# Optimization experiments

Measured on AMD Instinct MI355X. Metric: run time of the kernel, lower is better.

Reference implementation:

```python
import jax, jax.numpy as jnp
import numpy as np

N_SAMPLES = 32768
WS, STEP = 2048, 256
DILATIONS = (1, 2, 4, 8, 16, 32, 64, 1)
N_KEEP = 16
N_ROOMS = 8
N_ATOMS = 2048


def stft_mag(x):
    # x: (B, 1, N) -> magnitude spectrogram (B, 128, 1025)
    B = x.shape[0]
    xx = jnp.pad(x.reshape(B, -1), ((0, 0), (0, WS - STEP)))  # right-pad -> exactly N/STEP frames
    n_frames = N_SAMPLES // STEP  # 128
    idx = jnp.arange(n_frames)[:, None] * STEP + jnp.arange(WS)[None, :]
    frames = xx[:, idx] * jnp.hanning(WS)[None, None, :]  # (B, 128, 2048)
    return jnp.abs(jnp.fft.rfft(frames, axis=-1))


def fft_convolve(a, b):
    # linear convolution via zero-padding to 2N, sliced back to N
    n = a.shape[-1]
    pad = [(0, 0)] * (a.ndim - 1) + [(0, n)]
    sa = jnp.fft.rfft(jnp.pad(a, pad), axis=-1)
    sb = jnp.fft.rfft(jnp.pad(b, pad), axis=-1)
    return jnp.fft.irfft(sa * sb, n=2 * n, axis=-1)[..., :n]


def mlp(z, w, b, g, be, ow, ob):
    # LinearOutputStack: (Linear -> LayerNorm -> leaky_relu) x3 -> Linear
    for i in range(w.shape[0]):
        z = z @ w[i] + b[i]
        mu = jnp.mean(z, -1, keepdims=True)
        var = jnp.var(z, -1, keepdims=True)
        z = (z - mu) / jnp.sqrt(var + 1e-5) * g[i] + be[i]
        z = jax.nn.leaky_relu(z, 0.2)
    return z @ ow + ob


def setup_inputs() -> dict:
    key = jax.random.key(0)
    ks = jax.random.split(key, 12)
    s = 0.02
    B = 4
    decay = jnp.linspace(1.0, 0.0, N_SAMPLES) ** 2
    atoms = jax.random.uniform(ks[0], (N_ATOMS, N_SAMPLES), minval=-0.01, maxval=0.01) * decay[None, :]
    imp = jax.random.normal(ks[1], (N_ROOMS, N_SAMPLES)) * (jnp.linspace(1.0, 0.0, N_SAMPLES) ** 4)[None, :]
    imp = imp / jnp.linalg.norm(imp, axis=-1, keepdims=True)
    return {
        'x': jax.random.normal(ks[2], (B, 1, N_SAMPLES)),
        'atoms': atoms,
        'enc_w': jax.random.normal(ks[3], (8, 1024, 1024, 2)) * s,
        'enc_b': jnp.zeros((8, 1024)),
        'up_w': jax.random.normal(ks[4], (256, 1024)) * s,
        'up_b': jnp.zeros((256,)),
        'lat_w': jax.random.normal(ks[5], (1024, 16)) * s,
        'lat_b': jnp.zeros((16,)),
        'room_w': jax.random.normal(ks[6], (3, 16, 16)) * s,
        'room_b': jnp.zeros((3, 16)),
        'room_g': jnp.ones((3, 16)),
        'room_be': jnp.zeros((3, 16)),
        'room_ow': jax.random.normal(ks[7], (16, N_ROOMS)) * s,
        'room_ob': jnp.zeros((N_ROOMS,)),
        'mix_w': jax.random.normal(ks[8], (3, 16, 16)) * s,
        'mix_b': jnp.zeros((3, 16)),
        'mix_g': jnp.ones((3, 16)),
        'mix_be': jnp.zeros((3, 16)),
        'mix_ow': jax.random.normal(ks[9], (16, 1)) * s,
        'mix_ob': jnp.zeros((1,)),
        'impulses': imp,
    }


def reference(x, atoms, enc_w, enc_b, up_w, up_b, lat_w, lat_b,
              room_w, room_b, room_g, room_be, room_ow, room_ob,
              mix_w, mix_b, mix_g, mix_be, mix_ow, mix_ob, impulses):
    B = x.shape[0]
    # ---- encode ----
    spec = stft_mag(x)[..., :1024]                    # (B, 128, 1024)
    h = jnp.transpose(spec, (0, 2, 1))                # (B, 1024, 128)
    for i, d in enumerate(DILATIONS):                  # anti-causal dilated residual stack
        y = jnp.pad(h, ((0, 0), (0, 0), (0, d)))      # pad the FUTURE
        y = jax.lax.conv_general_dilated(y, enc_w[i], (1,), 'VALID', rhs_dilation=(d,),
                                         dimension_numbers=('NCH', 'OIH', 'NCH'))
        h = h + jax.nn.leaky_relu(y + enc_b[i][None, :, None], 0.2)
    z = jnp.mean(h, axis=-1)                          # (B, 1024)
    dense = z @ lat_w + lat_b                          # (B, 16)
    dense = dense / (jnp.linalg.norm(dense, axis=-1, keepdims=True) + 1e-8)  # unit_norm
    # ---- generate ----
    enc = jnp.einsum('bct,oc->bot', h, up_w) + up_b[None, :, None]  # 1x1 conv -> (B, 256, 128)
    full = jnp.zeros((B, 256, N_SAMPLES), enc.dtype).at[:, :, ::STEP].set(enc)
    # sparsify2: flattened top-k over (channel, time)
    flat = full.reshape(B, -1)
    vals, idx = jax.lax.top_k(flat, N_KEEP)           # (B, 16)
    ch = idx // N_SAMPLES                              # atom/channel index per event
    t = idx % N_SAMPLES                                # time index per event
    packed = jnp.zeros((B, N_KEEP, N_SAMPLES), full.dtype).at[
        jnp.arange(B)[:, None], jnp.arange(N_KEEP)[None, :], t].set(vals)
    subset = atoms[ch]                                 # gather -> (B, 16, 32768)
    events = fft_convolve(packed, subset)              # (B, 16, N)
    dry = jnp.sum(events, axis=1, keepdims=True)       # (B, 1, N)
    # ---- reverb ----
    room = jax.nn.softmax(mlp(dense, room_w, room_b, room_g, room_be, room_ow, room_ob), axis=-1)
    impulse = room @ impulses                          # (B, N)
    wet = fft_convolve(dry, impulse[:, None, :])
    mix = jax.nn.sigmoid(mlp(dense, mix_w, mix_b, mix_g, mix_be, mix_ow, mix_ob))[:, :, None]  # (B,1,1)
    return dry * mix + wet * (1.0 - mix)
```

## Files before the change

kernel.cpp:

```cpp
#include <hip/hip_runtime.h>
#include <hip/hip_bf16.h>
#include <math.h>

#define NSMP 32768
#define NFR 128
#define NCH 1024
#define NB 4

typedef __attribute__((ext_vector_type(8))) short short8;
typedef __attribute__((ext_vector_type(4))) float f32x4;
typedef unsigned short ushort;

__device__ __forceinline__ void split_bf(float v, ushort& h, ushort& l) {
  __hip_bfloat16 bh = __float2bfloat16(v);
  float r = v - __bfloat162float(bh);
  __hip_bfloat16 bl = __float2bfloat16(r);
  h = *reinterpret_cast<ushort*>(&bh);
  l = *reinterpret_cast<ushort*>(&bl);
}

__device__ __forceinline__ void gload_lds16(const ushort* g, ushort* l) {
  __builtin_amdgcn_global_load_lds((const __attribute__((address_space(1))) void*)g,
                                   (__attribute__((address_space(3))) void*)l, 16, 0, 0);
}

__global__ __launch_bounds__(256) void stft_kernel(const float* __restrict__ x,
                                                   float* __restrict__ h,
                                                   ushort* __restrict__ hTh,
                                                   ushort* __restrict__ hTl,
                                                   ushort* __restrict__ hTh1,
                                                   ushort* __restrict__ hTl1) {
  __shared__ float re[2048];
  __shared__ float im[2048];
  __shared__ float twr[1024];
  __shared__ float twi[1024];
  int bid = blockIdx.x;
  int b = bid >> 7;
  int f = bid & 127;
  int tid = threadIdx.x;
  const float TWO_PI = 6.28318530717958647692f;
  if (f < 64) {
    size_t pidx = ((size_t)b * 192 + 128 + f) * 1024 + tid * 4;
    uint2 z = {0u, 0u};
    *(uint2*)&hTh[pidx] = z;  *(uint2*)&hTl[pidx] = z;
    *(uint2*)&hTh1[pidx] = z; *(uint2*)&hTl1[pidx] = z;
  }
  for (int k = tid; k < 1024; k += 256) {
    float ang = -TWO_PI * (float)k / 2048.0f;
    float sn, cs;
    sincosf(ang, &sn, &cs);
    twr[k] = cs; twi[k] = sn;
  }
  for (int i = tid; i < 2048; i += 256) {
    int rev = (int)(__brev((unsigned)i) >> 21);
    int pos = f * 256 + rev;
    float v = (pos < NSMP) ? x[b * NSMP + pos] : 0.f;
    float w = 0.5f - 0.5f * cosf(TWO_PI * (float)rev / 2047.0f);
    re[i] = v * w;
    im[i] = 0.f;
  }
  __syncthreads();
  for (int s = 0; s < 11; ++s) {
    for (int q = 0; q < 4; ++q) {
      int bi = tid + q * 256;
      int half = 1 << s;
      int j = bi & (half - 1);
      int i0 = ((bi >> s) << (s + 1)) | j;
      int i1 = i0 + half;
      int ti = j << (10 - s);
      float cs = twr[ti], sn = twi[ti];
      float ur = re[i0], ui = im[i0];
      float vr = re[i1], vi = im[i1];
      float tr = vr * cs - vi * sn;
      float tti = vr * sn + vi * cs;
      re[i0] = ur + tr; im[i0] = ui + tti;
      re[i1] = ur - tr; im[i1] = ui - tti;
    }
    __syncthreads();
  }
  for (int k = tid; k < 1024; k += 256) {
    float m = sqrtf(re[k] * re[k] + im[k] * im[k]);
    h[(b * NCH + k) * NFR + f] = m;
    ushort hi, lo;
    split_bf(m, hi, lo);
    size_t tidx = ((size_t)b * 192 + f) * 1024 + k;
    hTh[tidx] = hi;
    hTl[tidx] = lo;
  }
}

__global__ __launch_bounds__(256) void wsplit_kernel(const float* __restrict__ encw,
                                                     ushort* __restrict__ w0h, ushort* __restrict__ w0l,
                                                     ushort* __restrict__ w1h, ushort* __restrict__ w1l) {
  size_t F = (size_t)blockIdx.x * 256 + threadIdx.x;
  float4 v = ((const float4*)encw)[F];
  size_t lo_idx = F >> 9;
  int c0 = (int)(F & 511) * 2;
  size_t base = lo_idx * 1024 + c0;
  ushort h0, l0, h1, l1;
  split_bf(v.x, h0, l0);
  split_bf(v.z, h1, l1);
  *(ushort2*)&w0h[base] = (ushort2){h0, h1};
  *(ushort2*)&w0l[base] = (ushort2){l0, l1};
  split_bf(v.y, h0, l0);
  split_bf(v.w, h1, l1);
  *(ushort2*)&w1h[base] = (ushort2){h0, h1};
  *(ushort2*)&w1l[base] = (ushort2){l0, l1};
}

__global__ __launch_bounds__(256) void conv_mfma(const ushort* __restrict__ hTh,
                                                 const ushort* __restrict__ hTl,
                                                 const ushort* __restrict__ w0h, const ushort* __restrict__ w0l,
                                                 const ushort* __restrict__ w1h, const ushort* __restrict__ w1l,
                                                 int D, float* __restrict__ yp) {
  __shared__ ushort lds[49152];
  int tid = threadIdx.x;
  int og = blockIdx.x * 128;
  int b = blockIdx.y;
  int s = blockIdx.z;
  int wid = tid >> 6, lane = tid & 63;
  int wr = (wid >> 1) * 64, wc = (wid & 1) * 64;
  int lr = lane & 15, lk = lane >> 4;
  int srow = lane >> 2;
  int sgr = ((lane & 3) ^ ((lane >> 3) & 3)) * 8;

  f32x4 acc[4][4];
#pragma unroll
  for (int m = 0; m < 4; ++m)
#pragma unroll
    for (int n = 0; n < 4; ++n) acc[m][n] = (f32x4){0.f, 0.f, 0.f, 0.f};

  const ushort* hb_h = hTh + (size_t)b * 192 * 1024;
  const ushort* hb_l = hTl + (size_t)b * 192 * 1024;

  auto stage = [&](int buf, int p) {
    const ushort* Wh = (p < 4) ? w0h : w1h;
    const ushort* Wl = (p < 4) ? w0l : w1l;
    int rowoff = (p < 4) ? 0 : D;
    int c0 = s * 128 + (p & 3) * 32 + sgr;
    ushort* dbase = &lds[buf * 16384 + wid * 4096];
#pragma unroll
    for (int j = 0; j < 8; ++j) {
      int row = j * 16 + srow;
      const ushort* src;
      if (wid == 0)      src = Wh   + (size_t)(og + row) * 1024 + c0;
      else if (wid == 1) src = Wl   + (size_t)(og + row) * 1024 + c0;
      else if (wid == 2) src = hb_h + (size_t)(rowoff + row) * 1024 + c0;
      else               src = hb_l + (size_t)(rowoff + row) * 1024 + c0;
      gload_lds16(src, dbase + j * 512);
    }
  };

  auto compute = [&](int buf) {
    const ushort* base = &lds[buf * 16384];
    short8 ah[4], al[4], bh[4], bl[4];
#pragma unroll
    for (int m = 0; m < 4; ++m) {
      int ar = wr + m * 16 + lr;
      int off = ar * 32 + ((lk ^ ((ar >> 1) & 3)) << 3);
      ah[m] = *(const short8*)&base[off];
      al[m] = *(const short8*)&base[4096 + off];
    }
#pragma unroll
    for (int n = 0; n < 4; ++n) {
      int br = wc + n * 16 + lr;
      int off = br * 32 + ((lk ^ ((br >> 1) & 3)) << 3);
      bh[n] = *(const short8*)&base[8192 + off];
      bl[n] = *(const short8*)&base[12288 + off];
    }
#pragma unroll
    for (int m = 0; m < 4; ++m)
#pragma unroll
      for (int n = 0; n < 4; ++n) {
        acc[m][n] = __builtin_amdgcn_mfma_f32_16x16x32_bf16(ah[m], bh[n], acc[m][n], 0, 0, 0);
        acc[m][n] = __builtin_amdgcn_mfma_f32_16x16x32_bf16(ah[m], bl[n], acc[m][n], 0, 0, 0);
        acc[m][n] = __builtin_amdgcn_mfma_f32_16x16x32_bf16(al[m], bh[n], acc[m][n], 0, 0, 0);
      }
  };

  stage(0, 0);
  stage(1, 1);
#pragma unroll
  for (int p = 0; p < 8; ++p) {
    if (p < 7) asm volatile("s_waitcnt vmcnt(8)" ::: "memory");
    else       asm volatile("s_waitcnt vmcnt(0)" ::: "memory");
    __builtin_amdgcn_s_barrier();
    if (p + 2 < 8) stage((p + 2) % 3, p + 2);
    compute(p % 3);
  }

  float* dst = yp + (size_t)(s * 4 + b) * 131072;
#pragma unroll
  for (int m = 0; m < 4; ++m)
#pragma unroll
    for (int n = 0; n < 4; ++n)
#pragma unroll
      for (int r = 0; r < 4; ++r) {
        int orow = og + wr + m * 16 + lk * 4 + r;
        int col = wc + n * 16 + lr;
        dst[orow * 128 + col] = acc[m][n][r];
      }
}

__global__ __launch_bounds__(256) void conv_epi(const float* __restrict__ yp,
                                                const float* __restrict__ hin,
                                                const float* __restrict__ bias,
                                                float* __restrict__ hout,
                                                ushort* __restrict__ hTh,
                                                ushort* __restrict__ hTl,
                                                float* __restrict__ zbuf) {
  __shared__ float T[16][132];
  int og = blockIdx.x * 16;
  int b = blockIdx.y;
  int tid = threadIdx.x;
#pragma unroll
  for (int j = 0; j < 8; ++j) {
    int flat = j * 256 + tid;
    int o = flat >> 7, t = flat & 127;
    size_t base = ((size_t)b * NCH + og + o) * NFR + t;
    float v = 0.f;
#pragma unroll
    for (int sl = 0; sl < 8; ++sl) v += yp[(size_t)sl * 524288 + base];
    v += bias[og + o];
    v = (v > 0.f) ? v : 0.2f * v;
    float r = hin[base] + v;
    hout[base] = r;
    T[o][t] = r;
  }
  __syncthreads();
  if (tid < 16) {
    float s = 0.f;
#pragma unroll 8
    for (int t = 0; t < 128; ++t) s += T[tid][t];
    zbuf[b * NCH + og + tid] = s * (1.f / 128.f);
  }
#pragma unroll
  for (int j = 0; j < 8; ++j) {
    int flat = j * 256 + tid;
    int t = flat >> 4, o = flat & 15;
    ushort hi, lo;
    split_bf(T[o][t], hi, lo);
    size_t tidx = ((size_t)b * 192 + t) * 1024 + og + o;
    hTh[tidx] = hi;
    hTl[tidx] = lo;
  }
}

template <int TAPS, int D, int KTOT, int SPLIT, int MROWS>
__global__ __launch_bounds__(256, 2) void gemm_f32(const float* __restrict__ hin,
                                                   const float* __restrict__ W,
                                                   float* __restrict__ yp) {
  __shared__ float As[64][68];
  __shared__ float Bs[64][132];
  int tid = threadIdx.x;
  int og = blockIdx.x * 64;
  int b = blockIdx.y;
  int s = blockIdx.z;
  const float* hb = hin + (size_t)b * (NCH * NFR);
  int tx = tid & 15;
  int ty = tid >> 4;
  float acc[4][8] = {};
  const int KS = KTOT / SPLIT;
  for (int kt = 0; kt < KS / 64; ++kt) {
    int k0 = s * KS + kt * 64;
    __syncthreads();
    {
      int r = tid >> 2;
      int seg = (tid & 3) * 16;
      const float4* src = (const float4*)(W + (size_t)(og + r) * KTOT + k0 + seg);
#pragma unroll
      for (int q = 0; q < 4; ++q) {
        float4 v = src[q];
        int row = seg + 4 * q;
#pragma unroll
        for (int i = 0; i < 4; ++i) {
          int rr = row + i;
          int col = r ^ (((rr >> 4) & 1) << 2);
          float val = (i == 0) ? v.x : (i == 1) ? v.y : (i == 2) ? v.z : v.w;
          As[rr][col] = val;
        }
      }
    }
    {
      int r = tid >> 2;
      int tq = (tid & 3) * 32;
      int c = k0 + r;
      const float4* src = (const float4*)(hb + (size_t)c * NFR + tq);
#pragma unroll
      for (int q = 0; q < 8; ++q) *(float4*)&Bs[r][tq + 4 * q] = src[q];
    }
    __syncthreads();
#pragma unroll 8
    for (int kk = 0; kk < 64; ++kk) {
      int ca = (ty * 4) ^ (((kk >> 4) & 1) << 2);
      float4 a0 = *(const float4*)&As[kk][ca];
      float4 b0 = *(const float4*)&Bs[kk][tx * 4];
      float4 b1 = *(const float4*)&Bs[kk][tx * 4 + 64];
      float av[4] = {a0.x, a0.y, a0.z, a0.w};
      float bv[8] = {b0.x, b0.y, b0.z, b0.w, b1.x, b1.y, b1.z, b1.w};
#pragma unroll
      for (int i = 0; i < 4; ++i)
#pragma unroll
        for (int j = 0; j < 8; ++j)
          acc[i][j] += av[i] * bv[j];
    }
  }
  float* ypb = yp + (size_t)s * (NB * MROWS * NFR) + (size_t)b * MROWS * NFR;
#pragma unroll
  for (int i = 0; i < 4; ++i) {
    int o = og + ty * 4 + i;
    *(float4*)&ypb[o * NFR + tx * 4] = (float4){acc[i][0], acc[i][1], acc[i][2], acc[i][3]};
    *(float4*)&ypb[o * NFR + tx * 4 + 64] = (float4){acc[i][4], acc[i][5], acc[i][6], acc[i][7]};
  }
}

__global__ void encsum_kernel(const float* __restrict__ ep, const float* __restrict__ upb,
                              float* __restrict__ enc) {
  int b = blockIdx.y;
  int i4 = blockIdx.x * 256 + threadIdx.x;
  int i = i4 * 4;
  float bv = upb[i >> 7];
  float4 s = {bv, bv, bv, bv};
#pragma unroll
  for (int sl = 0; sl < 16; ++sl) {
    float4 p = *(const float4*)&ep[(size_t)sl * 131072 + b * 32768 + i];
    s.x += p.x; s.y += p.y; s.z += p.z; s.w += p.w;
  }
  *(float4*)&enc[b * 32768 + i] = s;
}

__global__ __launch_bounds__(64) void dense_mlp_kernel(
    const float* __restrict__ zbuf,
    const float* __restrict__ latw, const float* __restrict__ latb,
    const float* __restrict__ rw, const float* __restrict__ rb,
    const float* __restrict__ rg, const float* __restrict__ rbe,
    const float* __restrict__ rowt, const float* __restrict__ rob,
    const float* __restrict__ mw, const float* __restrict__ mb,
    const float* __restrict__ mg, const float* __restrict__ mbe,
    const float* __restrict__ mow, const float* __restrict__ mob,
    float* __restrict__ room, float* __restrict__ mixv) {
  int b = blockIdx.x;
  int tid = threadIdx.x;
  const float* z = zbuf + b * NCH;
  int j = tid & 15;
  int p = tid >> 4;
  float dsum = 0.f;
  for (int c = p * 256; c < p * 256 + 256; ++c)
    dsum += z[c] * latw[c * 16 + j];
  dsum += __shfl_xor(dsum, 16);
  dsum += __shfl_xor(dsum, 32);
  float dj = dsum + latb[j];
  float sq = dj * dj;
  sq += __shfl_xor(sq, 1, 16);
  sq += __shfl_xor(sq, 2, 16);
  sq += __shfl_xor(sq, 4, 16);
  sq += __shfl_xor(sq, 8, 16);
  float a = dj / (sqrtf(sq) + 1e-8f);

  const float* W = rw;  const float* Bb = rb;
  const float* G = rg;  const float* Be = rbe;
  for (int which = 0; which < 2; ++which) {
    float v = a;
    for (int l = 0; l < 3; ++l) {
      float accv = Bb[l * 16 + j];
      for (int k = 0; k < 16; ++k) {
        float ak = __shfl(v, (tid & 48) | k);
        accv += ak * W[(l * 16 + k) * 16 + j];
      }
      float mu = accv;
      mu += __shfl_xor(mu, 1, 16); mu += __shfl_xor(mu, 2, 16);
      mu += __shfl_xor(mu, 4, 16); mu += __shfl_xor(mu, 8, 16);
      mu *= (1.f / 16.f);
      float dv = accv - mu;
      float var = dv * dv;
      var += __shfl_xor(var, 1, 16); var += __shfl_xor(var, 2, 16);
      var += __shfl_xor(var, 4, 16); var += __shfl_xor(var, 8, 16);
      var *= (1.f / 16.f);
      float xn = dv * rsqrtf(var + 1e-5f) * G[l * 16 + j] + Be[l * 16 + j];
      v = (xn > 0.f) ? xn : 0.2f * xn;
    }
    if (which == 0) {
      int r = tid & 7;
      float logit = rob[r];
      for (int k = 0; k < 16; ++k) {
        float ak = __shfl(v, (tid & 48) | k);
        logit += ak * rowt[k * 8 + r];
      }
      float mx = logit;
      mx = fmaxf(mx, __shfl_xor(mx, 1, 8));
      mx = fmaxf(mx, __shfl_xor(mx, 2, 8));
      mx = fmaxf(mx, __shfl_xor(mx, 4, 8));
      float e = expf(logit - mx);
      float se = e;
      se += __shfl_xor(se, 1, 8);
      se += __shfl_xor(se, 2, 8);
      se += __shfl_xor(se, 4, 8);
      if (tid < 8) room[b * 8 + r] = e / se;
      W = mw; Bb = mb; G = mg; Be = mbe;
    } else {
      float logit = mob[0];
      for (int k = 0; k < 16; ++k) {
        float ak = __shfl(v, (tid & 48) | k);
        logit += ak * mow[k];
      }
      if (tid == 0) mixv[b] = 1.f / (1.f + expf(-logit));
    }
  }
}

__global__ __launch_bounds__(256) void topk_kernel(const float* __restrict__ enc,
                                                   float* __restrict__ vals,
                                                   int* __restrict__ chs,
                                                   int* __restrict__ tps) {
  __shared__ float swv[4];
  __shared__ int swi[4];
  int b = blockIdx.x;
  int tid = threadIdx.x;
  const float* e = enc + b * 32768;
  float lv[16];
  int li[16];
#pragma unroll
  for (int q = 0; q < 16; ++q) { lv[q] = -INFINITY; li[q] = 0x7fffffff; }
  for (int i = tid; i < 32768; i += 256) {
    float v = e[i];
    if (v > lv[15]) {
      float cv = v; int ci = i;
#pragma unroll
      for (int q = 0; q < 16; ++q) {
        if (cv > lv[q]) {
          float tv = lv[q]; int ti = li[q];
          lv[q] = cv; li[q] = ci;
          cv = tv; ci = ti;
        }
      }
    }
  }
  for (int round = 0; round < 16; ++round) {
    float cv = lv[0];
    int ci = li[0];
#pragma unroll
    for (int off = 1; off < 64; off <<= 1) {
      float ov = __shfl_xor(cv, off);
      int oi = __shfl_xor(ci, off);
      if (ov > cv || (ov == cv && oi < ci)) { cv = ov; ci = oi; }
    }
    if ((tid & 63) == 0) { swv[tid >> 6] = cv; swi[tid >> 6] = ci; }
    __syncthreads();
    float wv = swv[0]; int wi = swi[0];
#pragma unroll
    for (int w = 1; w < 4; ++w) {
      float v2 = swv[w]; int i2 = swi[w];
      if (v2 > wv || (v2 == wv && i2 < wi)) { wv = v2; wi = i2; }
    }
    if (tid == 0) {
      vals[b * 16 + round] = (wv > 0.f) ? wv : 0.f;
      chs[b * 16 + round] = wi >> 7;
      tps[b * 16 + round] = (wi & 127) * 256;
    }
    if (li[0] == wi) {
#pragma unroll
      for (int q = 0; q < 15; ++q) { lv[q] = lv[q + 1]; li[q] = li[q + 1]; }
      lv[15] = -INFINITY; li[15] = 0x7fffffff;
    }
    __syncthreads();
  }
}

__global__ void dryimp_kernel(const float* __restrict__ atoms,
                              const float* __restrict__ vals, const int* __restrict__ chs,
                              const int* __restrict__ tps, const float* __restrict__ imps,
                              const float* __restrict__ room,
                              float* __restrict__ dry, float* __restrict__ imp) {
  int b = blockIdx.y;
  int n = blockIdx.x * 256 + threadIdx.x;
  float acc = 0.f;
#pragma unroll 4
  for (int j = 0; j < 16; ++j) {
    float v = vals[b * 16 + j];
    int tp = tps[b * 16 + j];
    int ch = chs[b * 16 + j];
    if (v != 0.f && n >= tp)
      acc += v * atoms[(size_t)ch * NSMP + (n - tp)];
  }
  dry[b * NSMP + n] = acc;
  float ia = 0.f;
#pragma unroll
  for (int r = 0; r < 8; ++r)
    ia += room[b * 8 + r] * imps[r * NSMP + n];
  imp[b * NSMP + n] = ia;
}

#define IS(a) is[(a) + ((a) >> 5)]
__global__ __launch_bounds__(256) void wet_kernel(const float* __restrict__ dry,
                                                  const float* __restrict__ impulse,
                                                  float* __restrict__ wp) {
  int s = blockIdx.x;
  int nt = blockIdx.y;
  int b = blockIdx.z;
  if (s > nt) return;
  __shared__ float is[4224];
  __shared__ float dsr[2048];
  int tid = threadIdx.x;
  int n0 = nt * 2048;
  int m0 = s * 2048;
  int base = n0 - m0 - 2047;
  const float* impb = impulse + b * NSMP;
  for (int k = tid; k < 4096; k += 256) {
    int idx = base + k;
    IS(k) = (idx >= 0 && idx < NSMP) ? impb[idx] : 0.f;
  }
  for (int i = tid; i < 2048; i += 256)
    dsr[i] = dry[b * NSMP + m0 + 2047 - i];
  __syncthreads();
  int aw = tid * 8;
  float w[8];
#pragma unroll
  for (int j = 0; j < 8; ++j) w[j] = IS(aw + j);
  float acc[8] = {};
  for (int jb = 0; jb < 2048; jb += 8) {
    float4 d0 = *(const float4*)&dsr[jb];
    float4 d1 = *(const float4*)&dsr[jb + 4];
    float dv[8] = {d0.x, d0.y, d0.z, d0.w, d1.x, d1.y, d1.z, d1.w};
#pragma unroll
    for (int e = 0; e < 8; ++e) {
      float dval = dv[e];
#pragma unroll
      for (int i = 0; i < 8; ++i)
        acc[i] += dval * w[(e + i) & 7];
      w[e] = IS(aw + jb + e + 8);
    }
  }
  float* dst = wp + (size_t)s * (NB * NSMP) + (size_t)b * NSMP + n0 + aw;
  *(float4*)dst = (float4){acc[0], acc[1], acc[2], acc[3]};
  *(float4*)(dst + 4) = (float4){acc[4], acc[5], acc[6], acc[7]};
}

__global__ void out_kernel(const float* __restrict__ dry, const float* __restrict__ wp,
                           const float* __restrict__ mixv, float* __restrict__ out) {
  int b = blockIdx.y;
  int n = blockIdx.x * 256 + threadIdx.x;
  float m = mixv[b];
  float wv = 0.f;
  int smax = n >> 11;
  for (int s = 0; s <= smax; ++s)
    wv += wp[(size_t)s * (NB * NSMP) + b * NSMP + n];
  out[b * NSMP + n] = dry[b * NSMP + n] * m + wv * (1.f - m);
}

extern "C" void kernel_launch(void* const* d_in, const int* in_sizes, int n_in,
                              void* d_out, int out_size, void* d_ws, size_t ws_size,
                              hipStream_t stream) {
  const float* x    = (const float*)d_in[0];
  const float* atoms= (const float*)d_in[1];
  const float* encw = (const float*)d_in[2];
  const float* encb = (const float*)d_in[3];
  const float* upw  = (const float*)d_in[4];
  const float* upb  = (const float*)d_in[5];
  const float* latw = (const float*)d_in[6];
  const float* latb = (const float*)d_in[7];
  const float* rw   = (const float*)d_in[8];
  const float* rb   = (const float*)d_in[9];
  const float* rg   = (const float*)d_in[10];
  const float* rbe  = (const float*)d_in[11];
  const float* rowt = (const float*)d_in[12];
  const float* rob  = (const float*)d_in[13];
  const float* mw   = (const float*)d_in[14];
  const float* mb   = (const float*)d_in[15];
  const float* mg   = (const float*)d_in[16];
  const float* mbe  = (const float*)d_in[17];
  const float* mow  = (const float*)d_in[18];
  const float* mob  = (const float*)d_in[19];
  const float* imps = (const float*)d_in[20];

  float* f    = (float*)d_ws;
  float* h0   = f;
  float* h1   = f + 524288;
  float* yp   = f + 1048576;
  float* ep   = yp;
  float* wp   = yp + 524288;
  float* dry  = f + 5242880;
  float* imp  = f + 5373952;
  float* encf = f + 5505024;
  float* room = f + 5636096;
  float* mixv = f + 5636128;
  float* vals = f + 5636160;
  int*   chs  = (int*)(f + 5636224);
  int*   tps  = (int*)(f + 5636288);
  float* zbuf = f + 5636352;
  ushort* w0h  = (ushort*)(f + 6000000);
  ushort* w0l  = w0h + 8388608;
  ushort* w1h  = w0l + 8388608;
  ushort* w1l  = w1h + 8388608;
  ushort* hTh0 = w1l + 8388608;
  ushort* hTl0 = hTh0 + 786432;
  ushort* hTh1 = hTl0 + 786432;
  ushort* hTl1 = hTh1 + 786432;

  wsplit_kernel<<<16384, 256, 0, stream>>>(encw, w0h, w0l, w1h, w1l);
  stft_kernel<<<512, 256, 0, stream>>>(x, h0, hTh0, hTl0, hTh1, hTl1);

  float* bufs[2] = {h0, h1};
  ushort* hThb[2] = {hTh0, hTh1};
  ushort* hTlb[2] = {hTl0, hTl1};
  const int dil[8] = {1, 2, 4, 8, 16, 32, 64, 1};
  for (int l = 0; l < 8; ++l) {
    int pi = l & 1, po = (l + 1) & 1;
    conv_mfma<<<dim3(8, 4, 8), 256, 0, stream>>>(
        hThb[pi], hTlb[pi],
        w0h + (size_t)l * 1048576, w0l + (size_t)l * 1048576,
        w1h + (size_t)l * 1048576, w1l + (size_t)l * 1048576,
        dil[l], yp);
    conv_epi<<<dim3(64, 4), 256, 0, stream>>>(yp, bufs[pi], encb + l * 1024,
                                              bufs[po], hThb[po], hTlb[po], zbuf);
  }

  dense_mlp_kernel<<<4, 64, 0, stream>>>(zbuf, latw, latb, rw, rb, rg, rbe, rowt, rob,
                                         mw, mb, mg, mbe, mow, mob, room, mixv);
  gemm_f32<1, 0, 1024, 16, 256><<<dim3(4, 4, 16), 256, 0, stream>>>(h0, upw, ep);
  encsum_kernel<<<dim3(32, 4), 256, 0, stream>>>(ep, upb, encf);
  topk_kernel<<<4, 256, 0, stream>>>(encf, vals, chs, tps);
  dryimp_kernel<<<dim3(128, 4), 256, 0, stream>>>(atoms, vals, chs, tps, imps, room, dry, imp);
  wet_kernel<<<dim3(16, 16, 4), 256, 0, stream>>>(dry, imp, wp);
  out_kernel<<<dim3(128, 4), 256, 0, stream>>>(dry, wp, mixv, (float*)d_out);
}
```

Baseline: 500.2 us.

## Fuse eight conv layers and epilogues into one persistent kernel with grid barriers

Replaces the 16 separate conv_mfma/conv_epi launches with a single persistent kernel of 256 blocks. Blocks synchronise through an atomic-counter grid barrier between the GEMM and epilogue phases of each layer. The goal is to remove per-launch overhead and the tail/drain gaps between layers. In exchange it relies on all 256 blocks being co-resident, which is not guaranteed by the launch, and it adds spin-wait barrier latency twice per layer.

After: 1.011 ms. +102.2%, slower.

```diff
diff --git a/kernel.cpp b/kernel.cpp
--- a/kernel.cpp
+++ b/kernel.cpp
@@ -22,6 +22,17 @@
 __device__ __forceinline__ void gload_lds16(const ushort* g, ushort* l) {
   __builtin_amdgcn_global_load_lds((const __attribute__((address_space(1))) void*)g,
                                    (__attribute__((address_space(3))) void*)l, 16, 0, 0);
+}
+
+__device__ __forceinline__ void gsync(unsigned* cnt, unsigned target) {
+  __syncthreads();
+  if (threadIdx.x == 0) {
+    __threadfence();
+    atomicAdd(cnt, 1u);
+    while (atomicAdd(cnt, 0u) < target) __builtin_amdgcn_s_sleep(2);
+    __threadfence();
+  }
+  __syncthreads();
 }
 
 __global__ __launch_bounds__(256) void stft_kernel(const float* __restrict__ x,
@@ -108,141 +119,165 @@
   *(ushort2*)&w1l[base] = (ushort2){l0, l1};
 }
 
-__global__ __launch_bounds__(256) void conv_mfma(const ushort* __restrict__ hTh,
-                                                 const ushort* __restrict__ hTl,
-                                                 const ushort* __restrict__ w0h, const ushort* __restrict__ w0l,
-                                                 const ushort* __restrict__ w1h, const ushort* __restrict__ w1l,
-                                                 int D, float* __restrict__ yp) {
+__global__ __launch_bounds__(256, 1) void conv_stack(
+    const ushort* __restrict__ w0hB, const ushort* __restrict__ w0lB,
+    const ushort* __restrict__ w1hB, const ushort* __restrict__ w1lB,
+    const float* __restrict__ encb,
+    float* __restrict__ h0, float* __restrict__ h1,
+    ushort* __restrict__ hTh0, ushort* __restrict__ hTl0,
+    ushort* __restrict__ hTh1, ushort* __restrict__ hTl1,
+    float* __restrict__ yp, float* __restrict__ zbuf,
+    unsigned* __restrict__ cnt) {
   __shared__ ushort lds[49152];
   int tid = threadIdx.x;
-  int og = blockIdx.x * 128;
-  int b = blockIdx.y;
-  int s = blockIdx.z;
+  int bid = blockIdx.x;
+  int og8 = bid >> 5;
+  int b = (bid >> 3) & 3;
+  int s = bid & 7;
+  int og = og8 * 128;
   int wid = tid >> 6, lane = tid & 63;
   int wr = (wid >> 1) * 64, wc = (wid & 1) * 64;
   int lr = lane & 15, lk = lane >> 4;
   int srow = lane >> 2;
   int sgr = ((lane & 3) ^ ((lane >> 3) & 3)) * 8;
 
-  f32x4 acc[4][4];
-#pragma unroll
-  for (int m = 0; m < 4; ++m)
-#pragma unroll
-    for (int n = 0; n < 4; ++n) acc[m][n] = (f32x4){0.f, 0.f, 0.f, 0.f};
-
-  const ushort* hb_h = hTh + (size_t)b * 192 * 1024;
-  const ushort* hb_l = hTl + (size_t)b * 192 * 1024;
-
-  auto stage = [&](int buf, int p) {
-    const ushort* Wh = (p < 4) ? w0h : w1h;
-    const ushort* Wl = (p < 4) ? w0l : w1l;
-    int rowoff = (p < 4) ? 0 : D;
-    int c0 = s * 128 + (p & 3) * 32 + sgr;
-    ushort* dbase = &lds[buf * 16384 + wid * 4096];
-#pragma unroll
-    for (int j = 0; j < 8; ++j) {
-      int row = j * 16 + srow;
-      const ushort* src;
-      if (wid == 0)      src = Wh   + (size_t)(og + row) * 1024 + c0;
-      else if (wid == 1) src = Wl   + (size_t)(og + row) * 1024 + c0;
-      else if (wid == 2) src = hb_h + (size_t)(rowoff + row) * 1024 + c0;
-      else               src = hb_l + (size_t)(rowoff + row) * 1024 + c0;
-      gload_lds16(src, dbase + j * 512);
-    }
-  };
-
-  auto compute = [&](int buf) {
-    const ushort* base = &lds[buf * 16384];
-    short8 ah[4], al[4], bh[4], bl[4];
-#pragma unroll
-    for (int m = 0; m < 4; ++m) {
-      int ar = wr + m * 16 + lr;
-      int off = ar * 32 + ((lk ^ ((ar >> 1) & 3)) << 3);
-      ah[m] = *(const short8*)&base[off];
-      al[m] = *(const short8*)&base[4096 + off];
-    }
-#pragma unroll
-    for (int n = 0; n < 4; ++n) {
-      int br = wc + n * 16 + lr;
-      int off = br * 32 + ((lk ^ ((br >> 1) & 3)) << 3);
-      bh[n] = *(const short8*)&base[8192 + off];
-      bl[n] = *(const short8*)&base[12288 + off];
-    }
+  const int dil[8] = {1, 2, 4, 8, 16, 32, 64, 1};
+  float* bufs[2] = {h0, h1};
+  ushort* thh[2] = {hTh0, hTh1};
+  ushort* thl[2] = {hTl0, hTl1};
+  unsigned target = 0;
+
+  for (int l = 0; l < 8; ++l) {
+    int D = dil[l];
+    const ushort* w0h = w0hB + (size_t)l * 1048576;
+    const ushort* w0l = w0lB + (size_t)l * 1048576;
+    const ushort* w1h = w1hB + (size_t)l * 1048576;
+    const ushort* w1l = w1lB + (size_t)l * 1048576;
+    int pi = l & 1, po = (l + 1) & 1;
+    const ushort* hb_h = thh[pi] + (size_t)b * 192 * 1024;
+    const ushort* hb_l = thl[pi] + (size_t)b * 192 * 1024;
+
+    f32x4 acc[4][4];
 #pragma unroll
     for (int m = 0; m < 4; ++m)
 #pragma unroll
+      for (int n = 0; n < 4; ++n) acc[m][n] = (f32x4){0.f, 0.f, 0.f, 0.f};
+
+    auto stage = [&](int buf, int p) {
+      const ushort* Wh = (p < 4) ? w0h : w1h;
+      const ushort* Wl = (p < 4) ? w0l : w1l;
+      int rowoff = (p < 4) ? 0 : D;
+      int c0 = s * 128 + (p & 3) * 32 + sgr;
+      ushort* dbase = &lds[buf * 16384 + wid * 4096];
+#pragma unroll
+      for (int j = 0; j < 8; ++j) {
+        int row = j * 16 + srow;
+        const ushort* src;
+        if (wid == 0)      src = Wh   + (size_t)(og + row) * 1024 + c0;
+        else if (wid == 1) src = Wl   + (size_t)(og + row) * 1024 + c0;
+        else if (wid == 2) src = hb_h + (size_t)(rowoff + row) * 1024 + c0;
+        else               src = hb_l + (size_t)(rowoff + row) * 1024 + c0;
+        gload_lds16(src, dbase + j * 512);
+      }
+    };
+
+    auto compute = [&](int buf) {
+      const ushort* base = &lds[buf * 16384];
+      short8 ah[4], al[4], bh[4], bl[4];
+#pragma unroll
+      for (int m = 0; m < 4; ++m) {
+        int ar = wr + m * 16 + lr;
+        int off = ar * 32 + ((lk ^ ((ar >> 1) & 3)) << 3);
+        ah[m] = *(const short8*)&base[off];
+        al[m] = *(const short8*)&base[4096 + off];
+      }
+#pragma unroll
       for (int n = 0; n < 4; ++n) {
-        acc[m][n] = __builtin_amdgcn_mfma_f32_16x16x32_bf16(ah[m], bh[n], acc[m][n], 0, 0, 0);
-        acc[m][n] = __builtin_amdgcn_mfma_f32_16x16x32_bf16(ah[m], bl[n], acc[m][n], 0, 0, 0);
-        acc[m][n] = __builtin_amdgcn_mfma_f32_16x16x32_bf16(al[m], bh[n], acc[m][n], 0, 0, 0);
-      }
-  };
-
-  stage(0, 0);
-  stage(1, 1);
-#pragma unroll
-  for (int p = 0; p < 8; ++p) {
-    if (p < 7) asm volatile("s_waitcnt vmcnt(8)" ::: "memory");
-    else       asm volatile("s_waitcnt vmcnt(0)" ::: "memory");
-    __builtin_amdgcn_s_barrier();
-    if (p + 2 < 8) stage((p + 2) % 3, p + 2);
-    compute(p % 3);
-  }
-
-  float* dst = yp + (size_t)(s * 4 + b) * 131072;
-#pragma unroll
-  for (int m = 0; m < 4; ++m)
-#pragma unroll
-    for (int n = 0; n < 4; ++n)
-#pragma unroll
-      for (int r = 0; r < 4; ++r) {
-        int orow = og + wr + m * 16 + lk * 4 + r;
-        int col = wc + n * 16 + lr;
-        dst[orow * 128 + col] = acc[m][n][r];
-      }
-}
-
-__global__ __launch_bounds__(256) void conv_epi(const float* __restrict__ yp,
-                                                const float* __restrict__ hin,
-                                                const float* __restrict__ bias,
-                                                float* __restrict__ hout,
-                                                ushort* __restrict__ hTh,
-                                                ushort* __restrict__ hTl,
-                                                float* __restrict__ zbuf) {
-  __shared__ float T[16][132];
-  int og = blockIdx.x * 16;
-  int b = blockIdx.y;
-  int tid = threadIdx.x;
-#pragma unroll
-  for (int j = 0; j < 8; ++j) {
-    int flat = j * 256 + tid;
-    int o = flat >> 7, t = flat & 127;
-    size_t base = ((size_t)b * NCH + og + o) * NFR + t;
-    float v = 0.f;
-#pragma unroll
-    for (int sl = 0; sl < 8; ++sl) v += yp[(size_t)sl * 524288 + base];
-    v += bias[og + o];
-    v = (v > 0.f) ? v : 0.2f * v;
-    float r = hin[base] + v;
-    hout[base] = r;
-    T[o][t] = r;
-  }
-  __syncthreads();
-  if (tid < 16) {
-    float s = 0.f;
+        int br = wc + n * 16 + lr;
+        int off = br * 32 + ((lk ^ ((br >> 1) & 3)) << 3);
+        bh[n] = *(const short8*)&base[8192 + off];
+        bl[n] = *(const short8*)&base[12288 + off];
+      }
+#pragma unroll
+      for (int m = 0; m < 4; ++m)
+#pragma unroll
+        for (int n = 0; n < 4; ++n) {
+          acc[m][n] = __builtin_amdgcn_mfma_f32_16x16x32_bf16(ah[m], bh[n], acc[m][n], 0, 0, 0);
+          acc[m][n] = __builtin_amdgcn_mfma_f32_16x16x32_bf16(ah[m], bl[n], acc[m][n], 0, 0, 0);
+          acc[m][n] = __builtin_amdgcn_mfma_f32_16x16x32_bf16(al[m], bh[n], acc[m][n], 0, 0, 0);
+        }
+    };
+
+    stage(0, 0);
+    stage(1, 1);
+#pragma unroll
+    for (int p = 0; p < 8; ++p) {
+      if (p < 7) asm volatile("s_waitcnt vmcnt(8)" ::: "memory");
+      else       asm volatile("s_waitcnt vmcnt(0)" ::: "memory");
+      __builtin_amdgcn_s_barrier();
+      if (p + 2 < 8) stage((p + 2) % 3, p + 2);
+      compute(p % 3);
+    }
+
+    {
+      float* dst = yp + (size_t)(s * 4 + b) * 131072;
+#pragma unroll
+      for (int m = 0; m < 4; ++m)
+#pragma unroll
+        for (int n = 0; n < 4; ++n)
+#pragma unroll
+          for (int r = 0; r < 4; ++r) {
+            int orow = og + wr + m * 16 + lk * 4 + r;
+            int col = wc + n * 16 + lr;
+            dst[orow * 128 + col] = acc[m][n][r];
+          }
+    }
+
+    target += 256;
+    gsync(cnt, target);
+
+    {
+      float* T = (float*)lds;
+      const float* hin = bufs[pi];
+      float* hout = bufs[po];
+      ushort* eTh = thh[po];
+      ushort* eTl = thl[po];
+      int oge = og + s * 16;
+#pragma unroll
+      for (int j = 0; j < 8; ++j) {
+        int flat = j * 256 + tid;
+        int o = flat >> 7, t = flat & 127;
+        size_t base = ((size_t)b * NCH + oge + o) * NFR + t;
+        float v = 0.f;
+#pragma unroll
+        for (int sl = 0; sl < 8; ++sl) v += yp[(size_t)sl * 524288 + base];
+        v += encb[l * NCH + oge + o];
+        v = (v > 0.f) ? v : 0.2f * v;
+        float r = hin[base] + v;
+        hout[base] = r;
+        T[o * 132 + t] = r;
+      }
+      __syncthreads();
+      if (tid < 16) {
+        float sm = 0.f;
 #pragma unroll 8
-    for (int t = 0; t < 128; ++t) s += T[tid][t];
-    zbuf[b * NCH + og + tid] = s * (1.f / 128.f);
-  }
-#pragma unroll
-  for (int j = 0; j < 8; ++j) {
-    int flat = j * 256 + tid;
-    int t = flat >> 4, o = flat & 15;
-    ushort hi, lo;
-    split_bf(T[o][t], hi, lo);
-    size_t tidx = ((size_t)b * 192 + t) * 1024 + og + o;
-    hTh[tidx] = hi;
-    hTl[tidx] = lo;
+        for (int t = 0; t < 128; ++t) sm += T[tid * 132 + t];
+        zbuf[b * NCH + oge + tid] = sm * (1.f / 128.f);
+      }
+#pragma unroll
+      for (int j = 0; j < 8; ++j) {
+        int flat = j * 256 + tid;
+        int t = flat >> 4, o = flat & 15;
+        ushort hi, lo;
+        split_bf(T[o * 132 + t], hi, lo);
+        size_t tidx = ((size_t)b * 192 + t) * 1024 + oge + o;
+        eTh[tidx] = hi;
+        eTl[tidx] = lo;
+      }
+    }
+
+    target += 256;
+    gsync(cnt, target);
   }
 }
 
@@ -587,6 +622,7 @@
   int*   chs  = (int*)(f + 5636224);
   int*   tps  = (int*)(f + 5636288);
   float* zbuf = f + 5636352;
+  unsigned* cnt = (unsigned*)(f + 5640448);
   ushort* w0h  = (ushort*)(f + 6000000);
   ushort* w0l  = w0h + 8388608;
   ushort* w1h  = w0l + 8388608;
@@ -596,23 +632,12 @@
   ushort* hTh1 = hTl0 + 786432;
   ushort* hTl1 = hTh1 + 786432;
 
+  hipMemsetAsync(cnt, 0, sizeof(unsigned), stream);
   wsplit_kernel<<<16384, 256, 0, stream>>>(encw, w0h, w0l, w1h, w1l);
   stft_kernel<<<512, 256, 0, stream>>>(x, h0, hTh0, hTl0, hTh1, hTl1);
 
-  float* bufs[2] = {h0, h1};
-  ushort* hThb[2] = {hTh0, hTh1};
-  ushort* hTlb[2] = {hTl0, hTl1};
-  const int dil[8] = {1, 2, 4, 8, 16, 32, 64, 1};
-  for (int l = 0; l < 8; ++l) {
-    int pi = l & 1, po = (l + 1) & 1;
-    conv_mfma<<<dim3(8, 4, 8), 256, 0, stream>>>(
-        hThb[pi], hTlb[pi],
-        w0h + (size_t)l * 1048576, w0l + (size_t)l * 1048576,
-        w1h + (size_t)l * 1048576, w1l + (size_t)l * 1048576,
-        dil[l], yp);
-    conv_epi<<<dim3(64, 4), 256, 0, stream>>>(yp, bufs[pi], encb + l * 1024,
-                                              bufs[po], hThb[po], hTlb[po], zbuf);
-  }
+  conv_stack<<<256, 256, 0, stream>>>(w0h, w0l, w1h, w1l, encb, h0, h1,
+                                      hTh0, hTl0, hTh1, hTl1, yp, zbuf, cnt);
 
   dense_mlp_kernel<<<4, 64, 0, stream>>>(zbuf, latw, latb, rw, rb, rg, rbe, rowt, rob,
                                          mw, mb, mg, mbe, mow, mob, room, mixv);
```

## Load MFMA operands directly from global memory instead of LDS pipeline

Applied to the files above, without the earlier changes.

Replaces the triple-buffered global_load_lds staging and barrier-synchronised LDS pipeline in the conv MFMA kernel with direct per-lane global loads of bf16 hi/lo fragments into registers. It drops the shared-memory footprint, the barriers and the waitcnt sequencing. In exchange, operands that several waves share are now fetched redundantly from global memory or cache, and there is no explicit prefetch overlap with the MFMA work. A local variable is also renamed in the epilogue kernel.

Result: slower. 563.1 us (+12.6%).

```diff
diff --git a/kernel.cpp b/kernel.cpp
--- a/kernel.cpp
+++ b/kernel.cpp
@@ -17,11 +17,6 @@
   __hip_bfloat16 bl = __float2bfloat16(r);
   h = *reinterpret_cast<ushort*>(&bh);
   l = *reinterpret_cast<ushort*>(&bl);
-}
-
-__device__ __forceinline__ void gload_lds16(const ushort* g, ushort* l) {
-  __builtin_amdgcn_global_load_lds((const __attribute__((address_space(1))) void*)g,
-                                   (__attribute__((address_space(3))) void*)l, 16, 0, 0);
 }
 
 __global__ __launch_bounds__(256) void stft_kernel(const float* __restrict__ x,
@@ -113,7 +108,6 @@
                                                  const ushort* __restrict__ w0h, const ushort* __restrict__ w0l,
                                                  const ushort* __restrict__ w1h, const ushort* __restrict__ w1l,
                                                  int D, float* __restrict__ yp) {
-  __shared__ ushort lds[49152];
   int tid = threadIdx.x;
   int og = blockIdx.x * 128;
   int b = blockIdx.y;
@@ -121,8 +115,6 @@
   int wid = tid >> 6, lane = tid & 63;
   int wr = (wid >> 1) * 64, wc = (wid & 1) * 64;
   int lr = lane & 15, lk = lane >> 4;
-  int srow = lane >> 2;
-  int sgr = ((lane & 3) ^ ((lane >> 3) & 3)) * 8;
 
   f32x4 acc[4][4];
 #pragma unroll
@@ -132,61 +124,38 @@
 
   const ushort* hb_h = hTh + (size_t)b * 192 * 1024;
   const ushort* hb_l = hTl + (size_t)b * 192 * 1024;
-
-  auto stage = [&](int buf, int p) {
-    const ushort* Wh = (p < 4) ? w0h : w1h;
-    const ushort* Wl = (p < 4) ? w0l : w1l;
-    int rowoff = (p < 4) ? 0 : D;
-    int c0 = s * 128 + (p & 3) * 32 + sgr;
-    ushort* dbase = &lds[buf * 16384 + wid * 4096];
-#pragma unroll
-    for (int j = 0; j < 8; ++j) {
-      int row = j * 16 + srow;
-      const ushort* src;
-      if (wid == 0)      src = Wh   + (size_t)(og + row) * 1024 + c0;
-      else if (wid == 1) src = Wl   + (size_t)(og + row) * 1024 + c0;
-      else if (wid == 2) src = hb_h + (size_t)(rowoff + row) * 1024 + c0;
-      else               src = hb_l + (size_t)(rowoff + row) * 1024 + c0;
-      gload_lds16(src, dbase + j * 512);
-    }
-  };
-
-  auto compute = [&](int buf) {
-    const ushort* base = &lds[buf * 16384];
-    short8 ah[4], al[4], bh[4], bl[4];
-#pragma unroll
-    for (int m = 0; m < 4; ++m) {
-      int ar = wr + m * 16 + lr;
-      int off = ar * 32 + ((lk ^ ((ar >> 1) & 3)) << 3);
-      ah[m] = *(const short8*)&base[off];
-      al[m] = *(const short8*)&base[4096 + off];
-    }
-#pragma unroll
-    for (int n = 0; n < 4; ++n) {
-      int br = wc + n * 16 + lr;
-      int off = br * 32 + ((lk ^ ((br >> 1) & 3)) << 3);
-      bh[n] = *(const short8*)&base[8192 + off];
-      bl[n] = *(const short8*)&base[12288 + off];
-    }
-#pragma unroll
-    for (int m = 0; m < 4; ++m)
+  int cbase = s * 128 + lk * 8;
+
+#pragma unroll
+  for (int tap = 0; tap < 2; ++tap) {
+    const ushort* Wh = tap ? w1h : w0h;
+    const ushort* Wl = tap ? w1l : w0l;
+    int rowoff = tap ? D : 0;
+#pragma unroll
+    for (int kc = 0; kc < 4; ++kc) {
+      int c0 = cbase + kc * 32;
+      short8 ah[4], al[4], bh[4], bl[4];
+#pragma unroll
+      for (int m = 0; m < 4; ++m) {
+        size_t off = (size_t)(og + wr + m * 16 + lr) * 1024 + c0;
+        ah[m] = *(const short8*)(Wh + off);
+        al[m] = *(const short8*)(Wl + off);
+      }
 #pragma unroll
       for (int n = 0; n < 4; ++n) {
-        acc[m][n] = __builtin_amdgcn_mfma_f32_16x16x32_bf16(ah[m], bh[n], acc[m][n], 0, 0, 0);
-        acc[m][n] = __builtin_amdgcn_mfma_f32_16x16x32_bf16(ah[m], bl[n], acc[m][n], 0, 0, 0);
-        acc[m][n] = __builtin_amdgcn_mfma_f32_16x16x32_bf16(al[m], bh[n], acc[m][n], 0, 0, 0);
-      }
-  };
-
-  stage(0, 0);
-  stage(1, 1);
-#pragma unroll
-  for (int p = 0; p < 8; ++p) {
-    if (p < 7) asm volatile("s_waitcnt vmcnt(8)" ::: "memory");
-    else       asm volatile("s_waitcnt vmcnt(0)" ::: "memory");
-    __builtin_amdgcn_s_barrier();
-    if (p + 2 < 8) stage((p + 2) % 3, p + 2);
-    compute(p % 3);
+        size_t off = (size_t)(wc + n * 16 + lr + rowoff) * 1024 + c0;
+        bh[n] = *(const short8*)(hb_h + off);
+        bl[n] = *(const short8*)(hb_l + off);
+      }
+#pragma unroll
+      for (int m = 0; m < 4; ++m)
+#pragma unroll
+        for (int n = 0; n < 4; ++n) {
+          acc[m][n] = __builtin_amdgcn_mfma_f32_16x16x32_bf16(ah[m], bh[n], acc[m][n], 0, 0, 0);
+          acc[m][n] = __builtin_amdgcn_mfma_f32_16x16x32_bf16(ah[m], bl[n], acc[m][n], 0, 0, 0);
+          acc[m][n] = __builtin_amdgcn_mfma_f32_16x16x32_bf16(al[m], bh[n], acc[m][n], 0, 0, 0);
+        }
+    }
   }
 
   float* dst = yp + (size_t)(s * 4 + b) * 131072;
@@ -229,10 +198,10 @@
   }
   __syncthreads();
   if (tid < 16) {
-    float s = 0.f;
+    float sm = 0.f;
 #pragma unroll 8
-    for (int t = 0; t < 128; ++t) s += T[tid][t];
-    zbuf[b * NCH + og + tid] = s * (1.f / 128.f);
+    for (int t = 0; t < 128; ++t) sm += T[tid][t];
+    zbuf[b * NCH + og + tid] = sm * (1.f / 128.f);
   }
 #pragma unroll
   for (int j = 0; j < 8; ++j) {
```
